# Kernel optimization log

Hardware: AMD Instinct MI355X
Metric: run time of the kernel (lower is better)

Reference implementation:

```python
import jax, jax.numpy as jnp
import numpy as np

# Dimensions: [B, head, ci_per_head, H, W]; rfft over last two dims.
B, H, CI, CO, S0, S1, M = 32, 8, 64, 64, 32, 64, 256
F1 = S1 // 2 + 1  # 33 rfft bins on last dim
SCALE = 1.0 / (512 * 512)  # 1/(in_channels*out_channels)


def setup_inputs() -> dict:
    key = jax.random.key(0)
    k1, k2, k3 = jax.random.split(key, 3)
    x = jax.random.normal(k1, (B, H, CI, S0, S1), dtype=jnp.float32)
    # torch.rand(..., dtype=cfloat) -> uniform[0,1) real and imag parts
    w_real = SCALE * jax.random.uniform(k2, (H, CI, CO, M), dtype=jnp.float32)
    w_imag = SCALE * jax.random.uniform(k3, (H, CI, CO, M), dtype=jnp.float32)
    # 'random' mode selection: 256 distinct flat indices into the S0*F1 rfft grid
    rng = np.random.default_rng(0)
    mask_idx = jnp.asarray(np.sort(rng.choice(S0 * F1, M, replace=False)).astype(np.int32))
    return {"x": x, "w_real": w_real, "w_imag": w_imag, "mask_idx": mask_idx}


def reference(x, w_real, w_imag, mask_idx):
    W = (w_real + 1j * w_imag).astype(jnp.complex64)  # (H, CI, CO, M)
    x_ft = jnp.fft.rfftn(x, axes=(3, 4), norm='ortho')  # (B,H,CI,S0,F1) complex64
    xf = x_ft.reshape(B, H, CI, S0 * F1)
    xm = jnp.take(xf, mask_idx, axis=-1)              # gather active modes (B,H,CI,M)
    om = jnp.einsum('bhil,hiol->bhol', xm, W)          # per-mode complex linear map
    out = jnp.zeros((B, H, CO, S0 * F1), dtype=jnp.complex64).at[..., mask_idx].set(om)
    out = out.reshape(B, H, CO, S0, F1)
    # canonical_fft_freq over freq dims except the rfft (last) dim: here only dim 3.
    # indexes/indexes2 form a full permutation pairing j <-> (-j) mod S0, so the
    # in-place averaging equals new[j] = (old[j] + conj(old[-j mod S0])) / 2.
    perm = (-jnp.arange(S0)) % S0
    out = 0.5 * (out + jnp.conj(out[:, :, :, perm, :]))
    y = jnp.fft.irfftn(out, s=(S0, S1), axes=(3, 4), norm='ortho')  # (B,H,CO,S0,S1) real
    return y
```

## Files before the change

### kernel.cpp

```cpp
#include <hip/hip_runtime.h>

#define F1 33

constexpr float TWD[64] = {
   1.00000000f,  0.99518473f,  0.98078528f,  0.95694034f,
   0.92387953f,  0.88192126f,  0.83146961f,  0.77301045f,
   0.70710678f,  0.63439328f,  0.55557023f,  0.47139674f,
   0.38268343f,  0.29028468f,  0.19509032f,  0.09801714f,
   0.00000000f, -0.09801714f, -0.19509032f, -0.29028468f,
  -0.38268343f, -0.47139674f, -0.55557023f, -0.63439328f,
  -0.70710678f, -0.77301045f, -0.83146961f, -0.88192126f,
  -0.92387953f, -0.95694034f, -0.98078528f, -0.99518473f,
  -1.00000000f, -0.99518473f, -0.98078528f, -0.95694034f,
  -0.92387953f, -0.88192126f, -0.83146961f, -0.77301045f,
  -0.70710678f, -0.63439328f, -0.55557023f, -0.47139674f,
  -0.38268343f, -0.29028468f, -0.19509032f, -0.09801714f,
   0.00000000f,  0.09801714f,  0.19509032f,  0.29028468f,
   0.38268343f,  0.47139674f,  0.55557023f,  0.63439328f,
   0.70710678f,  0.77301045f,  0.83146961f,  0.88192126f,
   0.92387953f,  0.95694034f,  0.98078528f,  0.99518473f,
};

#define NROWS 524288

__global__ __launch_bounds__(256) void k_sort(const int* __restrict__ mask,
                                              int* __restrict__ sorted,
                                              int* __restrict__ invperm) {
  __shared__ int ks[256];
  __shared__ int sv[256];
  __shared__ int skey[256];
  int t = threadIdx.x;
  int mi = mask[t];
  int j = mi / F1;
  int k = mi - j * F1;
  ks[t] = k;
  __syncthreads();
  int mykey = (k << 8) | t;
  int rank = 0;
  for (int l2 = 0; l2 < 256; ++l2)
    rank += (((ks[l2] << 8) | l2) < mykey);
  sv[rank]   = (k << 16) | (j << 8) | t;
  skey[rank] = k;
  invperm[t] = rank;
  __syncthreads();
  int isend = (t == 255) || (skey[t] != skey[t + 1]);
  sorted[t] = sv[t] | (isend << 24);
}

__global__ __launch_bounds__(256, 4) void k_fwd(const float* __restrict__ x,
                                                const int* __restrict__ sorted,
                                                float2* __restrict__ xm) {
  __shared__ float2 rbuf[128][35];
  __shared__ float2 cs32[32];
  int t = threadIdx.x;
  if (t < 32) cs32[t] = make_float2(TWD[(2 * t) & 63], TWD[(2 * t + 48) & 63]);

  int rl  = t >> 1;
  int par = t & 1;
  size_t row = (size_t)blockIdx.x * 128 + rl;
  const float4* xp = (const float4*)(x + row * 64);

  float f[32];
#pragma unroll
  for (int q = 0; q < 16; ++q) {
    float4 v = xp[q];
    f[2 * q + 0] = par ? v.y : v.x;
    f[2 * q + 1] = par ? v.w : v.z;
  }

  float s1v[16], d1v[16];
#pragma unroll
  for (int m = 0; m < 16; ++m) {
    s1v[m] = f[m] + f[m + 16];
    d1v[m] = f[m] - f[m + 16];
  }
  float s2v[8], d2v[8];
#pragma unroll
  for (int m = 0; m < 8; ++m) {
    s2v[m] = s1v[m] + s1v[m + 8];
    d2v[m] = s1v[m] - s1v[m + 8];
  }
  float mR[17], mI[17];
#pragma unroll
  for (int j = 0; j < 17; ++j) { mR[j] = 0.f; mI[j] = 0.f; }
#pragma unroll
  for (int m = 0; m < 8; ++m) {
#pragma unroll
    for (int tq = 0; tq < 5; ++tq) {
      const int j = 4 * tq;
      const int a = (2 * j * m) & 63;
      const float c  = TWD[a];
      const float sn = TWD[(a + 48) & 63];
      if (c  != 0.0f) mR[j] = fmaf(s2v[m],  c,  mR[j]);
      if (sn != 0.0f) mI[j] = fmaf(s2v[m], -sn, mI[j]);
    }
  }
#pragma unroll
  for (int m = 0; m < 8; ++m) {
#pragma unroll
    for (int tq = 0; tq < 4; ++tq) {
      const int j = 4 * tq + 2;
      const int a = (2 * j * m) & 63;
      const float c  = TWD[a];
      const float sn = TWD[(a + 48) & 63];
      if (c  != 0.0f) mR[j] = fmaf(d2v[m],  c,  mR[j]);
      if (sn != 0.0f) mI[j] = fmaf(d2v[m], -sn, mI[j]);
    }
  }
#pragma unroll
  for (int m = 0; m < 16; ++m) {
#pragma unroll
    for (int r = 0; r < 8; ++r) {
      const int j = 2 * r + 1;
      const int a = (2 * j * m) & 63;
      const float c  = TWD[a];
      const float sn = TWD[(a + 48) & 63];
      if (c  != 0.0f) mR[j] = fmaf(d1v[m],  c,  mR[j]);
      if (sn != 0.0f) mI[j] = fmaf(d1v[m], -sn, mI[j]);
    }
  }

  float oR[17], oI[17];
#pragma unroll
  for (int j = 0; j < 17; ++j) {
    oR[j] = __shfl_xor(mR[j], 1, 64);
    oI[j] = __shfl_xor(mI[j], 1, 64);
  }

  if (par == 0) {
#pragma unroll
    for (int k = 0; k <= 16; ++k) {
      const float wr = TWD[k];
      const float s  = TWD[(k + 48) & 63];
      float XR = mR[k];
      float XI = mI[k];
      if (s  != 0.0f) { XR = fmaf( s, oI[k], XR); XI = fmaf(-s, oR[k], XI); }
      if (wr != 0.0f) { XR = fmaf(wr, oR[k], XR); XI = fmaf(wr, oI[k], XI); }
      rbuf[rl][k] = make_float2(XR, XI);
    }
  } else {
#pragma unroll
    for (int k = 17; k <= 31; ++k) {
      const float wr = TWD[k];
      const float s  = TWD[(k + 48) & 63];
      const int p = 32 - k;
      float XR = oR[p];
      float XI = -oI[p];
      if (s  != 0.0f) { XR = fmaf(-s, mI[p], XR); XI = fmaf(-s, mR[p], XI); }
      if (wr != 0.0f) { XR = fmaf(wr, mR[p], XR); XI = fmaf(-wr, mI[p], XI); }
      rbuf[rl][k] = make_float2(XR, XI);
    }
    rbuf[rl][32] = make_float2(oR[0] - mR[0], 0.0f);
  }
  __syncthreads();

  int e = sorted[t];
  int k = (e >> 16) & 63, j = (e >> 8) & 255, l = e & 255;
  float2 acc[4];
#pragma unroll
  for (int u = 0; u < 4; ++u) acc[u] = make_float2(0.f, 0.f);

#pragma unroll 4
  for (int s0 = 0; s0 < 32; ++s0) {
    float2 cs = cs32[(j * s0) & 31];
#pragma unroll
    for (int u = 0; u < 4; ++u) {
      float2 rv = rbuf[u * 32 + s0][k];
      acc[u].x = fmaf(rv.x, cs.x, fmaf(rv.y,  cs.y, acc[u].x));
      acc[u].y = fmaf(rv.y, cs.x, fmaf(-rv.x, cs.y, acc[u].y));
    }
  }
  size_t ub = (size_t)blockIdx.x * 4;
#pragma unroll
  for (int u = 0; u < 4; ++u)
    xm[(ub + u) * 256 + l] = acc[u];
}

__global__ __launch_bounds__(512, 2) void k_mix(const float2* __restrict__ xm,
                                                const float* __restrict__ wr,
                                                const float* __restrict__ wi,
                                                float2* __restrict__ om) {
  __shared__ float4 Asm4[8][4][33];
  __shared__ float4 Wsm4[8][65][4];
  int t = threadIdx.x;
  int h  = blockIdx.x >> 5;
  int lb = (blockIdx.x & 31) * 8;

  int w    = t >> 6;
  int lane = t & 63;
  int b_lo = lane >> 2;
  int o_lo = lane & 3;

  float4 acc[2][2][4];
#pragma unroll
  for (int brp = 0; brp < 2; ++brp)
#pragma unroll
    for (int orp = 0; orp < 2; ++orp)
#pragma unroll
      for (int p = 0; p < 4; ++p)
        acc[brp][orp][p] = make_float4(0.f, 0.f, 0.f, 0.f);

  for (int ic = 0; ic < 8; ++ic) {
    __syncthreads();
#pragma unroll
    for (int q = 0; q < 2; ++q) {
      int c = t + 512 * q;
      int p = c & 3, ii = (c >> 2) & 7, b = c >> 5;
      const float4* src = (const float4*)(xm +
          (size_t)(((b * 8 + h) * 64) + ic * 8 + ii) * 256 + lb + 2 * p);
      Asm4[ii][p][b] = *src;
    }
#pragma unroll
    for (int q = 0; q < 2; ++q) {
      int c = t + 512 * q;
      int p2 = c & 1, oo = (c >> 1) & 63, ii = c >> 7;
      size_t gidx = (size_t)((h * 64 + ic * 8 + ii) * 64 + oo) * 256 + lb + p2 * 4;
      float4 vr = *(const float4*)(wr + gidx);
      float4 vi = *(const float4*)(wi + gidx);
      Wsm4[ii][oo][2 * p2 + 0] = make_float4(vr.x, vi.x, vr.y, vi.y);
      Wsm4[ii][oo][2 * p2 + 1] = make_float4(vr.z, vi.z, vr.w, vi.w);
    }
    __syncthreads();
#pragma unroll
    for (int i = 0; i < 8; ++i) {
      float4 av[2][4], wv[2][4];
#pragma unroll
      for (int brp = 0; brp < 2; ++brp)
#pragma unroll
        for (int p = 0; p < 4; ++p)
          av[brp][p] = Asm4[i][p][brp * 16 + b_lo];
#pragma unroll
      for (int orp = 0; orp < 2; ++orp)
#pragma unroll
        for (int p = 0; p < 4; ++p)
          wv[orp][p] = Wsm4[i][w * 8 + orp * 4 + o_lo][p];
#pragma unroll
      for (int brp = 0; brp < 2; ++brp)
#pragma unroll
        for (int orp = 0; orp < 2; ++orp)
#pragma unroll
          for (int p = 0; p < 4; ++p) {
            float4 A = av[brp][p], W = wv[orp][p];
            float4& C = acc[brp][orp][p];
            C.x = fmaf(A.x, W.x, fmaf(-A.y, W.y, C.x));
            C.y = fmaf(A.x, W.y, fmaf( A.y, W.x, C.y));
            C.z = fmaf(A.z, W.z, fmaf(-A.w, W.w, C.z));
            C.w = fmaf(A.z, W.w, fmaf( A.w, W.z, C.w));
          }
    }
  }
#pragma unroll
  for (int brp = 0; brp < 2; ++brp)
#pragma unroll
    for (int orp = 0; orp < 2; ++orp)
#pragma unroll
      for (int p = 0; p < 4; ++p) {
        int b = brp * 16 + b_lo;
        int o = w * 8 + orp * 4 + o_lo;
        *(float4*)(om + (size_t)(((b * 8 + h) * 64) + o) * 256 + lb + 2 * p)
            = acc[brp][orp][p];
      }
}

__global__ __launch_bounds__(256, 4) void k_inv_a(const float2* __restrict__ om,
                                                  const int* __restrict__ sorted,
                                                  const int* __restrict__ invperm,
                                                  float* __restrict__ T) {
  __shared__ float4 om16s[16 * 128];
  __shared__ float2 cs32[32];
  __shared__ int4   smodes4[64];
  int t = threadIdx.x;
  size_t ub = (size_t)blockIdx.x * 16;

  {
    int pos = invperm[t];
    float2* dst = (float2*)om16s;
    const float2* omg = om + ub * 256;
#pragma unroll
    for (int u = 0; u < 16; ++u)
      dst[u * 256 + pos] = omg[u * 256 + t];
  }
  if (t < 32) cs32[t] = make_float2(TWD[(2 * t) & 63], TWD[(2 * t + 48) & 63]);
  if (t < 64) smodes4[t] = ((const int4*)sorted)[t];
  __syncthreads();

  int up = t >> 5;
  int a  = t & 31;
  int u0 = up * 2, u1 = u0 + 1;
  float g0 = 0.f, g1 = 0.f;
  long long seen = 0;

#define PROC2(EV, R0, I0, R1, I1)                                             \
  do {                                                                        \
    int e_ = (EV);                                                            \
    int j_ = (e_ >> 8) & 255;                                                 \
    float2 cs_ = cs32[(j_ * a) & 31];                                         \
    g0 = fmaf((R0), cs_.x, g0); g0 = fmaf(-(I0), cs_.y, g0);                  \
    g1 = fmaf((R1), cs_.x, g1); g1 = fmaf(-(I1), cs_.y, g1);                  \
    if (e_ & (1 << 24)) {                                                     \
      int k_ = (e_ >> 16) & 63;                                               \
      seen |= 1ll << k_;                                                      \
      T[(size_t)k_ * NROWS + (ub + u0) * 32 + a] = g0;                        \
      T[(size_t)k_ * NROWS + (ub + u1) * 32 + a] = g1;                        \
      g0 = 0.f; g1 = 0.f;                                                     \
    }                                                                         \
  } while (0)

#pragma unroll 2
  for (int q = 0; q < 64; ++q) {
    int4   ee  = smodes4[q];
    float4 oA0 = om16s[u0 * 128 + 2 * q + 0];
    float4 oB0 = om16s[u0 * 128 + 2 * q + 1];
    float4 oA1 = om16s[u1 * 128 + 2 * q + 0];
    float4 oB1 = om16s[u1 * 128 + 2 * q + 1];
    PROC2(ee.x, oA0.x, oA0.y, oA1.x, oA1.y);
    PROC2(ee.y, oA0.z, oA0.w, oA1.z, oA1.w);
    PROC2(ee.z, oB0.x, oB0.y, oB1.x, oB1.y);
    PROC2(ee.w, oB0.z, oB0.w, oB1.z, oB1.w);
  }
#undef PROC2

#pragma unroll
  for (int k = 0; k < 33; ++k)
    if (!((seen >> k) & 1)) {
      T[(size_t)k * NROWS + (ub + u0) * 32 + a] = 0.f;
      T[(size_t)k * NROWS + (ub + u1) * 32 + a] = 0.f;
    }
}

template <int SG>
__device__ __forceinline__ void inv_b_body(const float (*T8)[34], int r,
                                           float* __restrict__ y, size_t Rb) {
  float acc[16];
  {
    float t0 = T8[r][0];
#pragma unroll
    for (int o = 0; o < 16; ++o)
      acc[o] = t0 * (1.0f / 2048.0f);
  }
#pragma unroll
  for (int k = 1; k < 33; ++k) {
    float tk = T8[r][k];
#pragma unroll
    for (int o = 0; o < 16; ++o) {
      const float C = ((k == 32) ? (1.0f / 2048.0f) : (2.0f / 2048.0f))
                    * TWD[(k * (SG * 16 + o)) & 63];
      if (C != 0.0f) acc[o] = fmaf(tk, C, acc[o]);
    }
  }
  float* yp = y + (Rb + r) * 64 + SG * 16;
#pragma unroll
  for (int q = 0; q < 4; ++q)
    *(float4*)(yp + 4 * q) = make_float4(acc[4 * q + 0], acc[4 * q + 1],
                                         acc[4 * q + 2], acc[4 * q + 3]);
}

__global__ __launch_bounds__(256, 4) void k_inv_b(const float* __restrict__ T,
                                                  float* __restrict__ y) {
  __shared__ float T8[64][34];
  int t = threadIdx.x;
  size_t Rb = (size_t)blockIdx.x * 64;

#pragma unroll
  for (int q = 0; q < 9; ++q) {
    int c = t + 256 * q;
    if (c < 2112) {
      int kq = c >> 6, r = c & 63;
      T8[r][kq] = T[(size_t)kq * NROWS + Rb + r];
    }
  }
  __syncthreads();

  int wv = t >> 6;
  int r  = t & 63;
  if      (wv == 0) inv_b_body<0>(T8, r, y, Rb);
  else if (wv == 1) inv_b_body<1>(T8, r, y, Rb);
  else if (wv == 2) inv_b_body<2>(T8, r, y, Rb);
  else              inv_b_body<3>(T8, r, y, Rb);
}

__global__ __launch_bounds__(512, 4) void k_inv(const float2* __restrict__ om,
                                                const int* __restrict__ sorted,
                                                const int* __restrict__ invperm,
                                                float* __restrict__ y) {
  __shared__ float4 om8s[8 * 128];
  __shared__ float  c2s[33][64];
  __shared__ float2 cs32[32];
  __shared__ int4   smodes4[64];
  int t = threadIdx.x;
  size_t ub = (size_t)blockIdx.x * 8;

  {
    int l  = t & 255;
    int u0 = t >> 8;
    int pos = invperm[l];
    float2* dst = (float2*)om8s;
    const float2* omg = om + ub * 256;
#pragma unroll
    for (int q = 0; q < 4; ++q) {
      int u = u0 + 2 * q;
      dst[u * 256 + pos] = omg[u * 256 + l];
    }
  }
#pragma unroll
  for (int q = 0; q < 5; ++q) {
    int idx = t + 512 * q;
    if (idx < 2112) {
      int k = idx >> 6, s1 = idx & 63;
      float w = (k == 0 || k == 32) ? (1.0f / 2048.0f) : (2.0f / 2048.0f);
      c2s[k][s1] = w * TWD[(k * s1) & 63];
    }
  }
  if (t < 32) cs32[t] = make_float2(TWD[(2 * t) & 63], TWD[(2 * t + 48) & 63]);
  if (t < 64) smodes4[t] = ((const int4*)sorted)[t];
  __syncthreads();

  int u    = t >> 6;
  int a    = (t >> 1) & 31;
  int half = t & 1;

  float4 a0 = make_float4(0.f,0.f,0.f,0.f), a1 = a0, a2 = a0, a3 = a0;
  float4 a4 = a0, a5 = a0, a6 = a0, a7 = a0;
  float g = 0.f;

#define SPREAD(KK)                                                            \
  do {                                                                        \
    const float4* crow = (const float4*)&c2s[(KK)][half * 32];                \
    float4 c;                                                                 \
    c = crow[0]; a0.x=fmaf(g,c.x,a0.x); a0.y=fmaf(g,c.y,a0.y); a0.z=fmaf(g,c.z,a0.z); a0.w=fmaf(g,c.w,a0.w); \
    c = crow[1]; a1.x=fmaf(g,c.x,a1.x); a1.y=fmaf(g,c.y,a1.y); a1.z=fmaf(g,c.z,a1.z); a1.w=fmaf(g,c.w,a1.w); \
    c = crow[2]; a2.x=fmaf(g,c.x,a2.x); a2.y=fmaf(g,c.y,a2.y); a2.z=fmaf(g,c.z,a2.z); a2.w=fmaf(g,c.w,a2.w); \
    c = crow[3]; a3.x=fmaf(g,c.x,a3.x); a3.y=fmaf(g,c.y,a3.y); a3.z=fmaf(g,c.z,a3.z); a3.w=fmaf(g,c.w,a3.w); \
    c = crow[4]; a4.x=fmaf(g,c.x,a4.x); a4.y=fmaf(g,c.y,a4.y); a4.z=fmaf(g,c.z,a4.z); a4.w=fmaf(g,c.w,a4.w); \
    c = crow[5]; a5.x=fmaf(g,c.x,a5.x); a5.y=fmaf(g,c.y,a5.y); a5.z=fmaf(g,c.z,a5.z); a5.w=fmaf(g,c.w,a5.w); \
    c = crow[6]; a6.x=fmaf(g,c.x,a6.x); a6.y=fmaf(g,c.y,a6.y); a6.z=fmaf(g,c.z,a6.z); a6.w=fmaf(g,c.w,a6.w); \
    c = crow[7]; a7.x=fmaf(g,c.x,a7.x); a7.y=fmaf(g,c.y,a7.y); a7.z=fmaf(g,c.z,a7.z); a7.w=fmaf(g,c.w,a7.w); \
    g = 0.f;                                                                  \
  } while (0)

#define PROC(EV, OVR, OVI)                                                    \
  do {                                                                        \
    int e_ = (EV);                                                            \
    int j_ = (e_ >> 8) & 255;                                                 \
    float2 cs_ = cs32[(j_ * a) & 31];                                         \
    g = fmaf((OVR), cs_.x, g);                                                \
    g = fmaf(-(OVI), cs_.y, g);                                               \
    if (e_ & (1 << 24)) SPREAD((e_ >> 16) & 63);                              \
  } while (0)

#pragma unroll 2
  for (int q = 0; q < 64; ++q) {
    int4   ee = smodes4[q];
    float4 oA = om8s[u * 128 + 2 * q + 0];
    float4 oB = om8s[u * 128 + 2 * q + 1];
    PROC(ee.x, oA.x, oA.y);
    PROC(ee.y, oA.z, oA.w);
    PROC(ee.z, oB.x, oB.y);
    PROC(ee.w, oB.z, oB.w);
  }
#undef PROC
#undef SPREAD

  float4* yp = (float4*)(y + (ub + u) * 2048 + a * 64 + half * 32);
  yp[0] = a0; yp[1] = a1; yp[2] = a2; yp[3] = a3;
  yp[4] = a4; yp[5] = a5; yp[6] = a6; yp[7] = a7;
}

extern "C" void kernel_launch(void* const* d_in, const int* in_sizes, int n_in,
                              void* d_out, int out_size, void* d_ws, size_t ws_size,
                              hipStream_t stream) {
  const float* x    = (const float*)d_in[0];
  const float* wre  = (const float*)d_in[1];
  const float* wim  = (const float*)d_in[2];
  const int*   mask = (const int*)d_in[3];

  float*  y  = (float*)d_out;
  float2* xm = (float2*)d_out;
  float2* omp = (float2*)d_ws;
  char* base = (char*)d_ws;
  int*  sorted  = (int*)(base + 33554432);
  int*  invperm = (int*)(base + 33555456);
  float* T      = (float*)(base + 33556480);
  const size_t ws_needed = 33556480ull + (size_t)33 * NROWS * 4;

  k_sort<<<1, 256, 0, stream>>>(mask, sorted, invperm);
  k_fwd <<<4096, 256, 0, stream>>>(x, sorted, xm);
  k_mix <<<256, 512, 0, stream>>>(xm, wre, wim, omp);
  if (ws_size >= ws_needed) {
    k_inv_a<<<1024, 256, 0, stream>>>(omp, sorted, invperm, T);
    k_inv_b<<<8192, 256, 0, stream>>>(T, y);
  } else {
    k_inv<<<2048, 512, 0, stream>>>(omp, sorted, invperm, y);
  }
}
```

Baseline: 227.9 us.

## Split k_mix input-channel reduction across two blocks and sum partials in inverse kernels

Splits the per-head input-channel reduction in k_mix into two halves, doubling the grid so more blocks occupy the GPU. Each half writes a partial result to its own buffer, one in workspace and one in spare output memory. The inverse kernels add the two partials while loading. This trades an extra partial-result write and read for more parallelism in the mixing stage.

```diff
diff --git a/kernel.cpp b/kernel.cpp
--- a/kernel.cpp
+++ b/kernel.cpp
@@ -179,12 +179,15 @@
 __global__ __launch_bounds__(512, 2) void k_mix(const float2* __restrict__ xm,
                                                 const float* __restrict__ wr,
                                                 const float* __restrict__ wi,
-                                                float2* __restrict__ om) {
+                                                float2* __restrict__ om0,
+                                                float2* __restrict__ om1) {
   __shared__ float4 Asm4[8][4][33];
   __shared__ float4 Wsm4[8][65][4];
   int t = threadIdx.x;
-  int h  = blockIdx.x >> 5;
-  int lb = (blockIdx.x & 31) * 8;
+  int ich = blockIdx.x >> 8;
+  int bh8 = blockIdx.x & 255;
+  int h  = bh8 >> 5;
+  int lb = (bh8 & 31) * 8;
 
   int w    = t >> 6;
   int lane = t & 63;
@@ -200,7 +203,7 @@
       for (int p = 0; p < 4; ++p)
         acc[brp][orp][p] = make_float4(0.f, 0.f, 0.f, 0.f);
 
-  for (int ic = 0; ic < 8; ++ic) {
+  for (int ic = ich * 4; ic < ich * 4 + 4; ++ic) {
     __syncthreads();
 #pragma unroll
     for (int q = 0; q < 2; ++q) {
@@ -249,6 +252,7 @@
           }
     }
   }
+  float2* __restrict__ omo = ich ? om1 : om0;
 #pragma unroll
   for (int brp = 0; brp < 2; ++brp)
 #pragma unroll
@@ -257,12 +261,13 @@
       for (int p = 0; p < 4; ++p) {
         int b = brp * 16 + b_lo;
         int o = w * 8 + orp * 4 + o_lo;
-        *(float4*)(om + (size_t)(((b * 8 + h) * 64) + o) * 256 + lb + 2 * p)
+        *(float4*)(omo + (size_t)(((b * 8 + h) * 64) + o) * 256 + lb + 2 * p)
             = acc[brp][orp][p];
       }
 }
 
-__global__ __launch_bounds__(256, 4) void k_inv_a(const float2* __restrict__ om,
+__global__ __launch_bounds__(256, 4) void k_inv_a(const float2* __restrict__ om0,
+                                                  const float2* __restrict__ om1,
                                                   const int* __restrict__ sorted,
                                                   const int* __restrict__ invperm,
                                                   float* __restrict__ T) {
@@ -275,10 +280,14 @@
   {
     int pos = invperm[t];
     float2* dst = (float2*)om16s;
-    const float2* omg = om + ub * 256;
-#pragma unroll
-    for (int u = 0; u < 16; ++u)
-      dst[u * 256 + pos] = omg[u * 256 + t];
+    const float2* omg0 = om0 + ub * 256;
+    const float2* omg1 = om1 + ub * 256;
+#pragma unroll
+    for (int u = 0; u < 16; ++u) {
+      float2 v0 = omg0[u * 256 + t];
+      float2 v1 = omg1[u * 256 + t];
+      dst[u * 256 + pos] = make_float2(v0.x + v1.x, v0.y + v1.y);
+    }
   }
   if (t < 32) cs32[t] = make_float2(TWD[(2 * t) & 63], TWD[(2 * t + 48) & 63]);
   if (t < 64) smodes4[t] = ((const int4*)sorted)[t];
@@ -379,7 +388,8 @@
   else              inv_b_body<3>(T8, r, y, Rb);
 }
 
-__global__ __launch_bounds__(512, 4) void k_inv(const float2* __restrict__ om,
+__global__ __launch_bounds__(512, 4) void k_inv(const float2* __restrict__ om0,
+                                                const float2* __restrict__ om1,
                                                 const int* __restrict__ sorted,
                                                 const int* __restrict__ invperm,
                                                 float* __restrict__ y) {
@@ -395,11 +405,14 @@
     int u0 = t >> 8;
     int pos = invperm[l];
     float2* dst = (float2*)om8s;
-    const float2* omg = om + ub * 256;
+    const float2* omg0 = om0 + ub * 256;
+    const float2* omg1 = om1 + ub * 256;
 #pragma unroll
     for (int q = 0; q < 4; ++q) {
       int u = u0 + 2 * q;
-      dst[u * 256 + pos] = omg[u * 256 + l];
+      float2 v0 = omg0[u * 256 + l];
+      float2 v1 = omg1[u * 256 + l];
+      dst[u * 256 + pos] = make_float2(v0.x + v1.x, v0.y + v1.y);
     }
   }
 #pragma unroll
@@ -476,8 +489,9 @@
 
   float*  y  = (float*)d_out;
   float2* xm = (float2*)d_out;
-  float2* omp = (float2*)d_ws;
+  float2* om1 = (float2*)d_out + 4194304;
   char* base = (char*)d_ws;
+  float2* om0   = (float2*)d_ws;
   int*  sorted  = (int*)(base + 33554432);
   int*  invperm = (int*)(base + 33555456);
   float* T      = (float*)(base + 33556480);
@@ -485,11 +499,11 @@
 
   k_sort<<<1, 256, 0, stream>>>(mask, sorted, invperm);
   k_fwd <<<4096, 256, 0, stream>>>(x, sorted, xm);
-  k_mix <<<256, 512, 0, stream>>>(xm, wre, wim, omp);
+  k_mix <<<512, 512, 0, stream>>>(xm, wre, wim, om0, om1);
   if (ws_size >= ws_needed) {
-    k_inv_a<<<1024, 256, 0, stream>>>(omp, sorted, invperm, T);
+    k_inv_a<<<1024, 256, 0, stream>>>(om0, om1, sorted, invperm, T);
     k_inv_b<<<8192, 256, 0, stream>>>(T, y);
   } else {
-    k_inv<<<2048, 512, 0, stream>>>(omp, sorted, invperm, y);
-  }
-}
+    k_inv<<<2048, 512, 0, stream>>>(om0, om1, sorted, invperm, y);
+  }
+}
```

Measured after the change: 238.3 us. 4.6% more time.
